# Optimization experiments

Hardware: AMD Instinct MI355X
Metric: run time of the kernel (lower is better)

The kernel has to match this reference:

```python
import jax, jax.numpy as jnp
import numpy as np

B, V, S, F, K = 4, 2048, 4, 16, 16
MAX_DISTANCE = jnp.finfo(jnp.float32).max


def setup_inputs() -> dict:
    key = jax.random.key(0)
    k1, k2, k3 = jax.random.split(key, 3)
    coordinates = jax.random.normal(k1, (B, V, S), dtype=jnp.float32)
    features = jax.random.normal(k2, (B, V, F), dtype=jnp.float32)
    # number of active vertices per event, in [V//2, V]
    active_vertices = jax.random.randint(k3, (B, 1), V // 2, V + 1, dtype=jnp.int32)
    return {"coordinates": coordinates, "features": features,
            "active_vertices": active_vertices}


def reference(coordinates, features, active_vertices):
    # raw_mask[i, j] = max(i, j); vertex pair (i, j) is valid iff max(i, j) < n_active
    idx = jnp.arange(V, dtype=jnp.int32)
    raw_mask = jnp.maximum(idx[None, :], idx[:, None])          # [V, V]
    mask = raw_mask[None, :, :] < active_vertices[:, :, None]    # [B, V, V]

    # pairwise Manhattan distance: [B, V, V]
    dist = jnp.sum(jnp.abs(coordinates[:, :, None, :] - coordinates[:, None, :, :]),
                   axis=-1)
    dist = jnp.where(mask, dist, MAX_DISTANCE)

    # top-k smallest distances (via top-k of negated distances)
    neg_ranked, ranked_idx = jax.lax.top_k(-dist, K)             # [B, V, K]
    neighbour_distances = -neg_ranked[:, :, 1:]                  # drop self: [B, V, K-1]
    neighbour_idx = ranked_idx[:, :, 1:]                         # [B, V, K-1]

    # gather neighbour features with batch dim: [B, V, K-1, F]
    batch_ix = jnp.arange(B, dtype=jnp.int32)[:, None, None]
    neighbour_features = features[batch_ix, neighbour_idx]

    return neighbour_distances, neighbour_features
```

## Files before the change

kernel.cpp:

```cpp
#include <hip/hip_runtime.h>

constexpr int B = 4, V = 2048, S = 4, F = 16, K = 16;
constexpr float MAXD = 3.4028234663852886e38f;
constexpr float BF16_SAFE_MAX = 3.3895313892515355e38f;
constexpr unsigned int INF_BITS = 0x7F800000u;


template <int CTRL>
__device__ __forceinline__ unsigned dppmov(unsigned x) {
  return (unsigned)__builtin_amdgcn_update_dpp((int)x, (int)x, CTRL, 0xF, 0xF, true);
}

template <int S_>
__device__ __forceinline__ void pair32(unsigned x, unsigned &u, unsigned &v) {
  if constexpr (S_ == 1) {
    u = x; v = dppmov<0xB1>(x);
  } else if constexpr (S_ == 2) {
    u = x; v = dppmov<0x4E>(x);
  } else if constexpr (S_ == 4) {
    u = x; v = (unsigned)__builtin_amdgcn_ds_swizzle((int)x, 0x101F);
  } else if constexpr (S_ == 8) {
    u = x; v = dppmov<0x128>(x);
  } else if constexpr (S_ == 16) {
#if __has_builtin(__builtin_amdgcn_permlane16_swap)
    auto r = __builtin_amdgcn_permlane16_swap(x, x, false, false);
    u = (unsigned)r[0]; v = (unsigned)r[1];
#else
    u = x; v = (unsigned)__builtin_amdgcn_ds_swizzle((int)x, 0x401F);
#endif
  } else {
#if __has_builtin(__builtin_amdgcn_permlane32_swap)
    auto r = __builtin_amdgcn_permlane32_swap(x, x, false, false);
    u = (unsigned)r[0]; v = (unsigned)r[1];
#else
    u = x; v = (unsigned)__shfl_xor((int)x, 32, 64);
#endif
  }
}

template <int S_>
__device__ __forceinline__ float ce_f32(float x, bool takemin) {
  unsigned u, v;
  pair32<S_>(__float_as_uint(x), u, v);
  const float a = __uint_as_float(u), b = __uint_as_float(v);
  const float mn = fminf(a, b), mx = fmaxf(a, b);
  return takemin ? mn : mx;
}

template <int S_>
__device__ __forceinline__ unsigned long long ce_u64(unsigned long long x,
                                                     bool takemin) {
  unsigned ul, vl, uh, vh;
  pair32<S_>((unsigned)x, ul, vl);
  pair32<S_>((unsigned)(x >> 32), uh, vh);
  const unsigned long long A = ((unsigned long long)uh << 32) | ul;
  const unsigned long long Bv = ((unsigned long long)vh << 32) | vl;
  const bool lt = A < Bv;
  const unsigned long long mn = lt ? A : Bv;
  const unsigned long long mx = lt ? Bv : A;
  return takemin ? mn : mx;
}

#define CEF(k_, s_) \
  sm = ce_f32<s_>(sm, (((lane & (k_)) == 0) == ((lane & (s_)) == 0)));
#define CEU(k_, s_) \
  key = ce_u64<s_>(key, (((lane & (k_)) == 0) == ((lane & (s_)) == 0)));

__global__ __launch_bounds__(256) void knn_kernel(
    const float* __restrict__ coords,
    const float* __restrict__ feats,
    const int*   __restrict__ act,
    float* __restrict__ out)
{
  __shared__ unsigned long long smem[4 * 64];

  const int lane = threadIdx.x & 63;
  const int wid  = (threadIdx.x >> 6) & 3;
  const int row  = (int)((blockIdx.x * blockDim.x + threadIdx.x) >> 6);
  const int b = row >> 11;
  const int i = row & (V - 1);
  const int a = act[b];

  float* out_d = out;
  float* out_f = out + (size_t)B * V * (K - 1);
  const float* fb = feats + (size_t)b * V * F;

  if (i >= a) {
    if (lane >= 1 && lane < K)
      out_d[(size_t)row * (K - 1) + (lane - 1)] = BF16_SAFE_MAX;
    const int n = (lane >> 2) + 1;
    const int part = lane & 3;
    if (lane < 60) {
      const float4 fv = *(const float4*)(fb + (size_t)n * F + part * 4);
      *(float4*)(out_f + ((size_t)row * (K - 1) + (n - 1)) * F + part * 4) = fv;
    }
    return;
  }

  const float* cb = coords + (size_t)b * V * S;
  const float4 ci = *(const float4*)(cb + i * 4);

  float d[32];
#pragma unroll
  for (int t = 0; t < 16; ++t) {
    const int j = t * 64 + lane;
    const float4 cj = *(const float4*)(cb + (size_t)j * 4);
    const float s0 = ci.x - cj.x, s1 = ci.y - cj.y;
    const float s2 = ci.z - cj.z, s3 = ci.w - cj.w;
    float dist = fabsf(s0) + fabsf(s1);
    dist += fabsf(s2);
    dist += fabsf(s3);
    d[t] = dist;
  }
#pragma unroll
  for (int t = 16; t < 32; ++t) {
    if (t * 64 < a) {
      const int j = t * 64 + lane;
      const float4 cj = *(const float4*)(cb + (size_t)j * 4);
      const float s0 = ci.x - cj.x, s1 = ci.y - cj.y;
      const float s2 = ci.z - cj.z, s3 = ci.w - cj.w;
      float dist = fabsf(s0) + fabsf(s1);
      dist += fabsf(s2);
      dist += fabsf(s3);
      d[t] = (j < a) ? dist : MAXD;
    } else {
      d[t] = MAXD;
    }
  }

  float u0 = fminf(fminf(d[0],  d[1]),  d[2]);
  float u1 = fminf(fminf(d[3],  d[4]),  d[5]);
  float u2 = fminf(fminf(d[6],  d[7]),  d[8]);
  float u3 = fminf(fminf(d[9],  d[10]), d[11]);
  float u4 = fminf(fminf(d[12], d[13]), d[14]);
  float u5 = fminf(fminf(d[15], d[16]), d[17]);
  float u6 = fminf(fminf(d[18], d[19]), d[20]);
  float u7 = fminf(fminf(d[21], d[22]), d[23]);
  float u8 = fminf(fminf(d[24], d[25]), d[26]);
  float u9 = fminf(fminf(d[27], d[28]), d[29]);
  float uA = fminf(d[30], d[31]);
  float w0 = fminf(fminf(u0, u1), u2);
  float w1 = fminf(fminf(u3, u4), u5);
  float w2 = fminf(fminf(u6, u7), u8);
  float w3 = fminf(u9, uA);
  const float m = fminf(fminf(fminf(w0, w1), w2), w3);

  float sm = m;
  CEF(2, 1)
  CEF(4, 2) CEF(4, 1)
  CEF(8, 4) CEF(8, 2) CEF(8, 1)
  CEF(16, 8) CEF(16, 4) CEF(16, 2) CEF(16, 1)
  CEF(32, 16) CEF(32, 8) CEF(32, 4) CEF(32, 2) CEF(32, 1)
  CEF(64, 32) CEF(64, 16) CEF(64, 8) CEF(64, 4) CEF(64, 2) CEF(64, 1)
  const float T = __uint_as_float(
      __builtin_amdgcn_readlane(__float_as_uint(sm), 16));

  int base = 0;
#pragma unroll
  for (int t = 0; t < 32; ++t) {
    const bool surv = (d[t] <= T);
    const unsigned long long mk = __ballot(surv);
    if (mk) {
      if (surv) {
        const int pos = base + (int)__builtin_amdgcn_mbcnt_hi(
                                   (unsigned)(mk >> 32),
                                   __builtin_amdgcn_mbcnt_lo((unsigned)mk, 0));
        const unsigned long long key =
            ((unsigned long long)__float_as_uint(d[t]) << 32) |
            (unsigned int)(t * 64 + lane);
        smem[wid * 64 + (pos < 64 ? pos : 63)] = key;
      }
      base += __popcll(mk);
    }
  }

  if (base <= 64) {
    unsigned long long key = 0xFFFFFFFFFFFFFFFFull;
    const unsigned long long v = smem[wid * 64 + lane];
    if (lane < base) key = v;
    CEU(2, 1)
    CEU(4, 2) CEU(4, 1)
    CEU(8, 4) CEU(8, 2) CEU(8, 1)
    CEU(16, 8) CEU(16, 4) CEU(16, 2) CEU(16, 1)
    CEU(32, 16) CEU(32, 8) CEU(32, 4) CEU(32, 2) CEU(32, 1)
    if (base > 32) {
      CEU(64, 32) CEU(64, 16) CEU(64, 8) CEU(64, 4) CEU(64, 2) CEU(64, 1)
    }
    if (lane >= 1 && lane < K) {
      const float wd = __uint_as_float((unsigned int)(key >> 32));
      out_d[(size_t)row * (K - 1) + (lane - 1)] = fminf(wd, BF16_SAFE_MAX);
    }
    const int myidx = (int)(key & 0xFFFFFFFFu);
    const int n = (lane >> 2) + 1;
    const int part = lane & 3;
    const int gidx = __shfl(myidx, n, 64);
    if (lane < 60) {
      const float4 fv = *(const float4*)(fb + (size_t)gidx * F + part * 4);
      *(float4*)(out_f + ((size_t)row * (K - 1) + (n - 1)) * F + part * 4) = fv;
    }
    return;
  }

  float my_dist = 0.0f;
  int   my_idx  = 0;
#pragma unroll
  for (int r = 0; r < K; ++r) {
    float bv = d[0];
    int   bt = 0;
#pragma unroll
    for (int t = 1; t < 32; ++t) {
      if (d[t] < bv) { bv = d[t]; bt = t; }
    }
    const unsigned int bidx = (unsigned int)(bt * 64 + lane);
    unsigned long long kk =
        ((unsigned long long)__float_as_uint(bv) << 32) | bidx;
#pragma unroll
    for (int s = 1; s < 64; s <<= 1) {
      const unsigned long long o = __shfl_xor(kk, s, 64);
      kk = (o < kk) ? o : kk;
    }
    const unsigned int widx  = (unsigned int)(kk & 0xFFFFFFFFu);
    const float        wdist = __uint_as_float((unsigned int)(kk >> 32));
    if (r > 0 && lane == r) { my_dist = wdist; my_idx = (int)widx; }
    if (r < K - 1) {
      const int  wl = (int)(widx & 63u);
      const int  wt = (int)(widx >> 6);
      const bool me = (lane == wl);
#pragma unroll
      for (int t = 0; t < 32; ++t) {
        if (me && (t == wt)) d[t] = __uint_as_float(INF_BITS);
      }
    }
  }
  if (lane >= 1 && lane < K) {
    out_d[(size_t)row * (K - 1) + (lane - 1)] = fminf(my_dist, BF16_SAFE_MAX);
  }
  const int n = (lane >> 2) + 1;
  const int part = lane & 3;
  const int gidx = __shfl(my_idx, n, 64);
  if (lane < 60) {
    const float4 fv = *(const float4*)(fb + (size_t)gidx * F + part * 4);
    *(float4*)(out_f + ((size_t)row * (K - 1) + (n - 1)) * F + part * 4) = fv;
  }
}

extern "C" void kernel_launch(void* const* d_in, const int* in_sizes, int n_in,
                              void* d_out, int out_size, void* d_ws, size_t ws_size,
                              hipStream_t stream) {
  const float* coords = (const float*)d_in[0];
  const float* feats  = (const float*)d_in[1];
  const int*   act    = (const int*)d_in[2];
  float* out = (float*)d_out;

  const int rows  = B * V;
  const int block = 256;
  const int grid  = rows * 64 / block;
  hipLaunchKernelGGL(knn_kernel, dim3(grid), dim3(block), 0, stream,
                     coords, feats, act, out);
}
```

Before: 21.61 us.

## Process two query rows per wavefront to reuse coordinate loads and balance work

Each wavefront now handles row i and row i+1024 of the same batch, so every coordinate load of candidate j serves two distance computations. Pairing a low-index row, which is always active, with a high-index row that may be inactive spreads the masked work evenly across wavefronts. The grid is halved and the selection logic is moved into a shared helper. In exchange, per-thread register use doubles (two 32-float distance arrays) and the two selections run one after the other, so occupancy and latency hiding may drop.

```diff
diff --git a/kernel.cpp b/kernel.cpp
--- a/kernel.cpp
+++ b/kernel.cpp
@@ -66,68 +66,11 @@
 #define CEU(k_, s_) \
   key = ce_u64<s_>(key, (((lane & (k_)) == 0) == ((lane & (s_)) == 0)));
 
-__global__ __launch_bounds__(256) void knn_kernel(
-    const float* __restrict__ coords,
-    const float* __restrict__ feats,
-    const int*   __restrict__ act,
-    float* __restrict__ out)
-{
-  __shared__ unsigned long long smem[4 * 64];
-
-  const int lane = threadIdx.x & 63;
-  const int wid  = (threadIdx.x >> 6) & 3;
-  const int row  = (int)((blockIdx.x * blockDim.x + threadIdx.x) >> 6);
-  const int b = row >> 11;
-  const int i = row & (V - 1);
-  const int a = act[b];
-
-  float* out_d = out;
-  float* out_f = out + (size_t)B * V * (K - 1);
-  const float* fb = feats + (size_t)b * V * F;
-
-  if (i >= a) {
-    if (lane >= 1 && lane < K)
-      out_d[(size_t)row * (K - 1) + (lane - 1)] = BF16_SAFE_MAX;
-    const int n = (lane >> 2) + 1;
-    const int part = lane & 3;
-    if (lane < 60) {
-      const float4 fv = *(const float4*)(fb + (size_t)n * F + part * 4);
-      *(float4*)(out_f + ((size_t)row * (K - 1) + (n - 1)) * F + part * 4) = fv;
-    }
-    return;
-  }
-
-  const float* cb = coords + (size_t)b * V * S;
-  const float4 ci = *(const float4*)(cb + i * 4);
-
-  float d[32];
-#pragma unroll
-  for (int t = 0; t < 16; ++t) {
-    const int j = t * 64 + lane;
-    const float4 cj = *(const float4*)(cb + (size_t)j * 4);
-    const float s0 = ci.x - cj.x, s1 = ci.y - cj.y;
-    const float s2 = ci.z - cj.z, s3 = ci.w - cj.w;
-    float dist = fabsf(s0) + fabsf(s1);
-    dist += fabsf(s2);
-    dist += fabsf(s3);
-    d[t] = dist;
-  }
-#pragma unroll
-  for (int t = 16; t < 32; ++t) {
-    if (t * 64 < a) {
-      const int j = t * 64 + lane;
-      const float4 cj = *(const float4*)(cb + (size_t)j * 4);
-      const float s0 = ci.x - cj.x, s1 = ci.y - cj.y;
-      const float s2 = ci.z - cj.z, s3 = ci.w - cj.w;
-      float dist = fabsf(s0) + fabsf(s1);
-      dist += fabsf(s2);
-      dist += fabsf(s3);
-      d[t] = (j < a) ? dist : MAXD;
-    } else {
-      d[t] = MAXD;
-    }
-  }
-
+__device__ __forceinline__ void select_and_emit(
+    const int lane, const int row, float (&d)[32],
+    unsigned long long* __restrict__ sreg,
+    const float* __restrict__ fb,
+    float* __restrict__ out_d, float* __restrict__ out_f) {
   float u0 = fminf(fminf(d[0],  d[1]),  d[2]);
   float u1 = fminf(fminf(d[3],  d[4]),  d[5]);
   float u2 = fminf(fminf(d[6],  d[7]),  d[8]);
@@ -168,7 +111,7 @@
         const unsigned long long key =
             ((unsigned long long)__float_as_uint(d[t]) << 32) |
             (unsigned int)(t * 64 + lane);
-        smem[wid * 64 + (pos < 64 ? pos : 63)] = key;
+        sreg[pos < 64 ? pos : 63] = key;
       }
       base += __popcll(mk);
     }
@@ -176,7 +119,7 @@
 
   if (base <= 64) {
     unsigned long long key = 0xFFFFFFFFFFFFFFFFull;
-    const unsigned long long v = smem[wid * 64 + lane];
+    const unsigned long long v = sreg[lane];
     if (lane < base) key = v;
     CEU(2, 1)
     CEU(4, 2) CEU(4, 1)
@@ -244,6 +187,99 @@
   }
 }
 
+__global__ __launch_bounds__(256, 4) void knn_kernel(
+    const float* __restrict__ coords,
+    const float* __restrict__ feats,
+    const int*   __restrict__ act,
+    float* __restrict__ out)
+{
+  __shared__ unsigned long long smem[8 * 64];
+
+  const int lane = threadIdx.x & 63;
+  const int wid  = (threadIdx.x >> 6) & 3;
+  const int gw   = blockIdx.x * 4 + wid;
+  const int b    = gw >> 10;
+  const int i1   = gw & 1023;
+  const int i2   = i1 + 1024;
+  const int row1 = b * V + i1;
+  const int row2 = b * V + i2;
+  const int a = __builtin_amdgcn_readfirstlane(act[b]);
+
+  float* out_d = out;
+  float* out_f = out + (size_t)B * V * (K - 1);
+  const float* fb = feats + (size_t)b * V * F;
+  const float* cb = coords + (size_t)b * V * S;
+
+  const float4 ci1 = *(const float4*)(cb + i1 * 4);
+  const float4 ci2 = *(const float4*)(cb + i2 * 4);
+  const bool r2_active = (i2 < a);
+
+  float d1[32], d2[32];
+#pragma unroll
+  for (int t = 0; t < 16; ++t) {
+    const int j = t * 64 + lane;
+    const float4 cj = *(const float4*)(cb + (size_t)j * 4);
+    {
+      const float s0 = ci1.x - cj.x, s1 = ci1.y - cj.y;
+      const float s2 = ci1.z - cj.z, s3 = ci1.w - cj.w;
+      float dist = fabsf(s0) + fabsf(s1);
+      dist += fabsf(s2);
+      dist += fabsf(s3);
+      d1[t] = dist;
+    }
+    {
+      const float s0 = ci2.x - cj.x, s1 = ci2.y - cj.y;
+      const float s2 = ci2.z - cj.z, s3 = ci2.w - cj.w;
+      float dist = fabsf(s0) + fabsf(s1);
+      dist += fabsf(s2);
+      dist += fabsf(s3);
+      d2[t] = dist;
+    }
+  }
+#pragma unroll
+  for (int t = 16; t < 32; ++t) {
+    if (t * 64 < a) {
+      const int j = t * 64 + lane;
+      const float4 cj = *(const float4*)(cb + (size_t)j * 4);
+      const bool valid = (j < a);
+      {
+        const float s0 = ci1.x - cj.x, s1 = ci1.y - cj.y;
+        const float s2 = ci1.z - cj.z, s3 = ci1.w - cj.w;
+        float dist = fabsf(s0) + fabsf(s1);
+        dist += fabsf(s2);
+        dist += fabsf(s3);
+        d1[t] = valid ? dist : MAXD;
+      }
+      {
+        const float s0 = ci2.x - cj.x, s1 = ci2.y - cj.y;
+        const float s2 = ci2.z - cj.z, s3 = ci2.w - cj.w;
+        float dist = fabsf(s0) + fabsf(s1);
+        dist += fabsf(s2);
+        dist += fabsf(s3);
+        d2[t] = valid ? dist : MAXD;
+      }
+    } else {
+      d1[t] = MAXD;
+      d2[t] = MAXD;
+    }
+  }
+
+  select_and_emit(lane, row1, d1, smem + (wid * 2 + 0) * 64, fb, out_d, out_f);
+
+  if (r2_active) {
+    select_and_emit(lane, row2, d2, smem + (wid * 2 + 1) * 64, fb, out_d, out_f);
+  } else {
+    if (lane >= 1 && lane < K)
+      out_d[(size_t)row2 * (K - 1) + (lane - 1)] = BF16_SAFE_MAX;
+    const int n = (lane >> 2) + 1;
+    const int part = lane & 3;
+    if (lane < 60) {
+      const float4 fv = *(const float4*)(fb + (size_t)n * F + part * 4);
+      *(float4*)(out_f + ((size_t)row2 * (K - 1) + (n - 1)) * F + part * 4) = fv;
+    }
+  }
+}
+
 extern "C" void kernel_launch(void* const* d_in, const int* in_sizes, int n_in,
                               void* d_out, int out_size, void* d_ws, size_t ws_size,
                               hipStream_t stream) {
@@ -252,9 +288,8 @@
   const int*   act    = (const int*)d_in[2];
   float* out = (float*)d_out;
 
-  const int rows  = B * V;
   const int block = 256;
-  const int grid  = rows * 64 / block;
+  const int grid  = (B * V / 2) * 64 / block;
   hipLaunchKernelGGL(knn_kernel, dim3(grid), dim3(block), 0, stream,
                      coords, feats, act, out);
 }
```

Result: slower. 47.94 us (+121.8%).
